# Optimization experiments

Measured on AMD Instinct MI355X. Metric: run time of the kernel, lower is better.

The kernel has to match this reference:

```python
import jax, jax.numpy as jnp
import numpy as np

N = 100_000      # atoms
E = 1_600_000    # edges (avg degree 16)
B = 50           # graphs in batch
H = 128          # hidden dim
R = 50           # num radial features (emb(0.0, 6.0, 50))
MAXZ = 100
CUTOFF = 6.0
L = 3            # interaction layers (ext[1..6])


def setup_inputs() -> dict:
    key = jax.random.key(0)
    ks = jax.random.split(key, 16)
    z = jax.random.randint(ks[0], (N,), 0, MAXZ)
    pos = jax.random.normal(ks[1], (N, 3), dtype=jnp.float32) * 3.0
    cell = jnp.eye(3, dtype=jnp.float32)[None] * 10.0 + 0.1 * jax.random.normal(ks[2], (B, 3, 3), dtype=jnp.float32)
    edge_index = jax.random.randint(ks[3], (2, E), 0, N)
    cell_offsets = jax.random.randint(ks[4], (E, 3), -1, 2)  # {-1,0,1}
    edge_batch = jax.random.randint(ks[5], (E,), 0, B)
    # learned parameters
    atom_emb = jax.random.normal(ks[6], (MAXZ, H), dtype=jnp.float32) * 0.1
    dist_table = jax.random.normal(ks[7], (R, R), dtype=jnp.float32) * 0.1  # dist_emb embedding table
    s_e = 1.0 / np.sqrt(2 * H + R)
    s_h = 1.0 / np.sqrt(H)
    We = jax.random.normal(ks[8], (L, 2 * H + R, H), dtype=jnp.float32) * s_e
    be = jnp.zeros((L, H), dtype=jnp.float32)
    Wv = jax.random.normal(ks[9], (L, H, H), dtype=jnp.float32) * s_h
    bv = jnp.zeros((L, H), dtype=jnp.float32)
    Wh = jax.random.normal(ks[10], (H, H), dtype=jnp.float32) * s_h
    bh = jnp.zeros((H,), dtype=jnp.float32)
    return dict(z=z, pos=pos, cell=cell, edge_index=edge_index,
                cell_offsets=cell_offsets, edge_batch=edge_batch,
                atom_emb=atom_emb, dist_table=dist_table,
                We=We, be=be, Wv=Wv, bv=bv, Wh=Wh, bh=bh)


def reference(z, pos, cell, edge_index, cell_offsets, edge_batch,
              atom_emb, dist_table, We, be, Wv, bv, Wh, bh):
    row, col = edge_index[0], edge_index[1]
    # get_pbc_distances: offsets = cell_offsets @ per-edge cell
    off = jnp.einsum('ek,ekl->el', cell_offsets.astype(jnp.float32), cell[edge_batch])  # [E,3]
    vec = pos[row] - pos[col] + off
    dist = jnp.sqrt(jnp.sum(vec * vec, axis=-1))  # [E]
    # dist_emb(dist.to(long)): integer-cast distance indexes the embedding table
    demb = dist_table[jnp.clip(dist.astype(jnp.int32), 0, R - 1)]  # [E,R]
    env = 0.5 * (jnp.cos(jnp.pi * jnp.clip(dist, 0.0, CUTOFF) / CUTOFF) + 1.0)  # cosine cutoff [E]
    v = atom_emb[z]  # ext[0]: atom embedding [N,H]
    for i in range(L):
        # ext[2i+1]: edge layer — gather endpoints, concat with radial features
        m = jnp.concatenate([v[row], v[col], demb], axis=-1)  # [E, 2H+R]
        e = jax.nn.silu(m @ We[i] + be[i]) * env[:, None]     # [E, H]
        # ext[2i+2]: node layer — scatter-sum messages to destination nodes
        agg = jax.ops.segment_sum(e, col, num_segments=N)     # [N, H]
        v = v + jax.nn.silu(agg @ Wv[i] + bv[i])
    v = v @ Wh + bh  # head
    return (v, pos, dist)
```

## Files before the change

kernel.cpp:

```cpp
#include <hip/hip_runtime.h>
#include <hip/hip_bf16.h>

#define HID 128
#define RR 50
#define NLAY 3
#define CBSH 9
#define CBSZ 512
#define CPAD (CBSZ * 3)
#define ACHUNK 8192

typedef __attribute__((ext_vector_type(8))) short short8;
typedef __attribute__((ext_vector_type(4))) float f32x4;
typedef __attribute__((ext_vector_type(2))) float f32x2;

static __device__ __forceinline__ unsigned short f2bf(float x) {
    unsigned int b = __builtin_bit_cast(unsigned int, x);
    b = b + 0x7FFFu + ((b >> 16) & 1u);
    return (unsigned short)(b >> 16);
}
static __device__ __forceinline__ float bf2f(unsigned int u) {
    return __builtin_bit_cast(float, u << 16);
}
static __device__ __forceinline__ f32x2 bfpair(unsigned u) {
    f32x2 r;
    r.x = __builtin_bit_cast(float, u << 16);
    r.y = __builtin_bit_cast(float, u & 0xffff0000u);
    return r;
}
static __device__ __forceinline__ float silu_f(float x) {
    float e = __expf(-x);
    return x * __builtin_amdgcn_rcpf(1.0f + e);
}

__global__ __launch_bounds__(256) void k_geom(
    const int* __restrict__ ei, const int* __restrict__ co,
    const int* __restrict__ eb, const float* __restrict__ cell,
    const float* __restrict__ pos, float* __restrict__ dist_out,
    int2* __restrict__ rec, int* __restrict__ ccol,
    float* __restrict__ out_pos, int N3, int E)
{
    int e = blockIdx.x * 256 + threadIdx.x;
    if (e < N3) out_pos[e] = pos[e];
    if (e >= E) return;
    int r = ei[e], c = ei[E + e], b = eb[e];
    float c0 = (float)co[3*e], c1 = (float)co[3*e+1], c2 = (float)co[3*e+2];
    const float* cb = cell + b * 9;
    float v0 = pos[3*r+0] - pos[3*c+0] + c0*cb[0] + c1*cb[3] + c2*cb[6];
    float v1 = pos[3*r+1] - pos[3*c+1] + c0*cb[1] + c1*cb[4] + c2*cb[7];
    float v2 = pos[3*r+2] - pos[3*c+2] + c0*cb[2] + c1*cb[5] + c2*cb[8];
    float d = sqrtf(v0*v0 + v1*v1 + v2*v2);
    dist_out[e] = d;
    bool keep = d < 6.0f;
    ccol[e] = keep ? c : -1;
    if (keep) {
        int di = (int)d;
        di = di < 0 ? 0 : (di > RR - 1 ? RR - 1 : di);
        float envv = 0.5f * (cosf(d * (3.14159265358979323846f / 6.0f)) + 1.0f);
        rec[e] = make_int2((r << 8) | di, __builtin_bit_cast(int, envv));
    }
}

__global__ __launch_bounds__(256) void k_cntA(
    const int* __restrict__ col, int* __restrict__ gb, int E, int nCB)
{
    __shared__ int lc[1024];
    int tid = threadIdx.x;
    for (int i = tid; i < nCB; i += 256) lc[i] = 0;
    __syncthreads();
    int base = blockIdx.x * ACHUNK;
    int end = base + ACHUNK; if (end > E) end = E;
    for (int e = base + tid; e < end; e += 256) {
        int c = col[e];
        if (c >= 0) atomicAdd(&lc[((unsigned)c) >> CBSH], 1);
    }
    __syncthreads();
    for (int i = tid; i < nCB; i += 256)
        if (lc[i]) atomicAdd(&gb[i], lc[i]);
}

__global__ __launch_bounds__(256) void k_projz(
    const int* __restrict__ z, const float* __restrict__ emb,
    const unsigned short* __restrict__ P12t,
    unsigned short* __restrict__ v, unsigned short* __restrict__ P1,
    unsigned short* __restrict__ P2, int N)
{
    int gid = blockIdx.x * 256 + threadIdx.x;
    if (gid >= N * 16) return;
    int n = gid >> 4, c4 = gid & 15;
    int zz = z[n];
    const float4* ep = (const float4*)(emb + (size_t)zz * HID) + c4 * 2;
    float4 a = ep[0], b = ep[1];
    uint4 u;
    u.x = ((unsigned)f2bf(a.y) << 16) | f2bf(a.x);
    u.y = ((unsigned)f2bf(a.w) << 16) | f2bf(a.z);
    u.z = ((unsigned)f2bf(b.y) << 16) | f2bf(b.x);
    u.w = ((unsigned)f2bf(b.w) << 16) | f2bf(b.z);
    *(uint4*)(v + (size_t)n * HID + c4 * 8) = u;
    uint4 t1 = *(const uint4*)(P12t + (size_t)zz * 256 + c4 * 8);
    uint4 t2 = *(const uint4*)(P12t + (size_t)zz * 256 + 128 + c4 * 8);
    *(uint4*)(P1 + (size_t)n * HID + c4 * 8) = t1;
    *(uint4*)(P2 + (size_t)n * HID + c4 * 8) = t2;
}

__global__ __launch_bounds__(256) void k_wprep(
    const float* __restrict__ We, const float* __restrict__ Wv,
    const float* __restrict__ Wh, const float* __restrict__ dt,
    const float* __restrict__ be, const float* __restrict__ emb,
    unsigned short* __restrict__ WvP, unsigned short* __restrict__ WcP,
    unsigned short* __restrict__ WhP, unsigned short* __restrict__ TbP,
    unsigned short* __restrict__ P12t)
{
    int blk = blockIdx.x;
    if (blk < 640) {
        int t = blk * 256 + threadIdx.x;
        int j = t & 7, l = (t >> 3) & 63, s = (t >> 9) & 3;
        int ln = l & 15, g = l >> 4;
        int k = s * 32 + g * 4 + (j & 3) + ((j >> 2) << 4);
        if (t < 3 * 16384) {
            int i = t >> 14; int nt = (t >> 11) & 7;
            WvP[t] = f2bf(Wv[(size_t)i * 16384 + k * HID + nt * 16 + ln]);
        } else if (t < 3 * 16384 + 3 * 32768) {
            int u = t - 3 * 16384; int i = u >> 15; int nt = (u >> 11) & 15;
            int col = nt * 16 + ln;
            float val = (col < HID) ? We[(size_t)i * 306 * HID + k * HID + col]
                                    : We[(size_t)i * 306 * HID + (HID + k) * HID + (col - HID)];
            WcP[u] = f2bf(val);
        } else {
            int u = t - 3 * 16384 - 3 * 32768; int nt = (u >> 11) & 7;
            WhP[u] = f2bf(Wh[k * HID + nt * 16 + ln]);
        }
    } else if (blk < 640 + NLAY * RR) {
        if (threadIdx.x >= HID) return;
        int row = blk - 640;
        int i = row / RR, r = row % RR;
        int c = threadIdx.x;
        float s = be[i * HID + c];
        const float* w = We + (size_t)i * 306 * HID + 256 * HID + c;
        const float* dr = dt + r * RR;
        for (int k = 0; k < RR; ++k) s += dr[k] * w[k * HID];
        TbP[(i * RR + r) * HID + c] = f2bf(s);
    } else {
        int zz = blk - 640 - NLAY * RR;
        int c = threadIdx.x;
        int cm = c & 127, half = c >> 7;
        const float* er = emb + (size_t)zz * HID;
        const float* w = We + (size_t)(half * 128) * HID + cm;
        float s = 0.f;
        #pragma unroll 8
        for (int k = 0; k < 128; ++k) s += er[k] * w[k * HID];
        P12t[(size_t)zz * 256 + c] = f2bf(s);
    }
}

__global__ __launch_bounds__(256) void k_scanA(
    const int* __restrict__ gb, int* __restrict__ gbase,
    int* __restrict__ gcur, int nCB)
{
    __shared__ int ps[256];
    __shared__ int carry;
    int t = threadIdx.x;
    if (t == 0) carry = 0;
    __syncthreads();
    for (int base = 0; base < nCB; base += 256) {
        int v = (base + t < nCB) ? gb[base + t] : 0;
        ps[t] = v; __syncthreads();
        for (int d = 1; d < 256; d <<= 1) {
            int x = (t >= d) ? ps[t - d] : 0;
            __syncthreads();
            ps[t] += x;
            __syncthreads();
        }
        int excl = carry + ps[t] - v;
        if (base + t < nCB) { gbase[base + t] = excl; gcur[base + t] = excl; }
        __syncthreads();
        if (t == 0) carry += ps[255];
        __syncthreads();
    }
    if (t == 0) gbase[nCB] = carry;
}

__global__ __launch_bounds__(256) void k_splitA(
    const int* __restrict__ col, const int2* __restrict__ rec,
    int* __restrict__ gcur, int2* __restrict__ binned,
    int* __restrict__ bcol, int E, int nCB)
{
    __shared__ int lc[1024];
    __shared__ int lres[1024];
    int tid = threadIdx.x;
    for (int i = tid; i < nCB; i += 256) lc[i] = 0;
    __syncthreads();
    int base = blockIdx.x * ACHUNK;
    int end = base + ACHUNK; if (end > E) end = E;
    for (int e = base + tid; e < end; e += 256) {
        int c = col[e];
        if (c >= 0) atomicAdd(&lc[((unsigned)c) >> CBSH], 1);
    }
    __syncthreads();
    for (int i = tid; i < nCB; i += 256) {
        lres[i] = lc[i] ? atomicAdd(&gcur[i], lc[i]) : 0;
        lc[i] = 0;
    }
    __syncthreads();
    for (int e = base + tid; e < end; e += 256) {
        int c = col[e];
        if (c < 0) continue;
        int b = ((unsigned)c) >> CBSH;
        int rank = atomicAdd(&lc[b], 1);
        int p = lres[b] + rank;
        binned[p] = rec[e];
        bcol[p] = c;
    }
}

__global__ __launch_bounds__(256) void k_sortB(
    const int2* __restrict__ binned, const int* __restrict__ bcol,
    const int* __restrict__ gbase, int2* __restrict__ meta,
    int2* __restrict__ noff, int N)
{
    __shared__ int lcnt[CBSZ], lcur[CBSZ], pscan[CBSZ];
    __shared__ int wsum[64];
    const int b = blockIdx.x;
    const int tid = threadIdx.x;
    const int s = gbase[b], e = gbase[b + 1];
    const int mbase = s + b * CPAD;
    for (int i = tid; i < CBSZ; i += 256) { lcnt[i] = 0; lcur[i] = 0; }
    __syncthreads();
    for (int t = s + tid; t < e; t += 256)
        atomicAdd(&lcnt[bcol[t] & (CBSZ - 1)], 1);
    __syncthreads();
    if (tid < 64) {
        int ssum = 0;
        #pragma unroll
        for (int k = 0; k < 8; ++k) {
            int idx = tid * 8 + k;
            int pc = (lcnt[idx] + 3) & ~3;
            pscan[idx] = ssum;
            ssum += pc;
        }
        wsum[tid] = ssum;
    }
    __syncthreads();
    if (tid == 0) {
        int c = 0;
        for (int i = 0; i < 64; ++i) { int t = wsum[i]; wsum[i] = c; c += t; }
    }
    __syncthreads();
    if (tid < 64) {
        #pragma unroll
        for (int k = 0; k < 8; ++k) pscan[tid * 8 + k] += wsum[tid];
    }
    __syncthreads();
    for (int i = tid; i < CBSZ; i += 256) {
        int node = (b << CBSH) + i;
        if (node < N) {
            noff[node] = make_int2(mbase + pscan[i], lcnt[i]);
            int pb = mbase + pscan[i] + lcnt[i];
            int pads = ((lcnt[i] + 3) & ~3) - lcnt[i];
            for (int k = 0; k < pads; ++k) meta[pb + k] = make_int2(0, 0);
        }
    }
    __syncthreads();
    for (int t = s + tid; t < e; t += 256) {
        int local = bcol[t] & (CBSZ - 1);
        int rank = atomicAdd(&lcur[local], 1);
        meta[mbase + pscan[local] + rank] = binned[t];
    }
}

#define PLD(M) (*(const unsigned*)(P1b + (unsigned)((((unsigned)(M).x) & 0xFFFFFF00u) | lane4)))
#define TLDG(M) (*(const unsigned*)(Tb_ + (((((unsigned)(M).x) & 255u) << 8) | lane4)))

#define EP(GG, TBU, MM)                                                       \
    {                                                                         \
        f32x2 xx = bfpair(GG) + (bfpair(TBU) + p2v);                          \
        f32x2 nx = xx * -1.442695041f;                                        \
        f32x2 ee;                                                             \
        ee.x = __builtin_amdgcn_exp2f(nx.x);                                  \
        ee.y = __builtin_amdgcn_exp2f(nx.y);                                  \
        f32x2 dd = ee + 1.0f;                                                 \
        f32x2 rr;                                                             \
        rr.x = __builtin_amdgcn_rcpf(dd.x);                                   \
        rr.y = __builtin_amdgcn_rcpf(dd.y);                                   \
        f32x2 sl = xx * rr;                                                   \
        float evf = __builtin_bit_cast(float, (MM).y);                        \
        av += sl * evf;                                                       \
    }

static __device__ __forceinline__ short8 ldfrag(const unsigned short* A, int r, int s, int g) {
    const char* p = (const char*)(A + r * 136) + s * 64 + g * 8;
    uint2 lo = *(const uint2*)p;
    uint2 hi = *(const uint2*)(p + 32);
    uint4 u; u.x = lo.x; u.y = lo.y; u.z = hi.x; u.w = hi.y;
    return __builtin_bit_cast(short8, u);
}

template<int NT2, bool FINAL>
__global__ __launch_bounds__(256) void k_layer(
    const unsigned short* __restrict__ P1,
    const unsigned short* __restrict__ P2,
    const unsigned short* __restrict__ TbBf,
    const int2* __restrict__ meta,
    const int2* __restrict__ noff,
    const unsigned short* __restrict__ B1p,
    const float* __restrict__ b1,
    unsigned short* __restrict__ v,
    const unsigned short* __restrict__ B2p,
    const float* __restrict__ b2,
    unsigned short* __restrict__ P1d,
    unsigned short* __restrict__ P2d,
    float* __restrict__ outd, int N)
{
    __shared__ __align__(16) unsigned short SHB[2 * 32 * 136];
    unsigned short* SH  = SHB;
    unsigned short* SHV = SHB + 32 * 136;
    const int tid = threadIdx.x;
    const int node0 = blockIdx.x * 32;
    const int w = tid >> 6, l = tid & 63, g = l >> 4, ln = l & 15;
    const int lane = l;
    const unsigned lane4 = 4u * (unsigned)lane;

    #pragma unroll
    for (int i = 0; i < 2; ++i) {
        int u = tid + 256 * i, r = u >> 4, c = u & 15;
        uint4 y4 = make_uint4(0, 0, 0, 0);
        if (node0 + r < N) y4 = *(const uint4*)(v + (size_t)(node0 + r) * HID + c * 8);
        *(uint4*)(SHV + r * 136 + c * 8) = y4;
    }

    {
        const char* P1b = (const char*)P1;
        const char* Tb_ = (const char*)TbBf;
        const int r0 = w << 3;
        int2 ni = make_int2(0, 0);
        {
            int pn = node0 + r0 + lane;
            if (lane < 8 && pn < N) ni = noff[pn];
        }
        #pragma unroll 1
        for (int i = 0; i < 8; ++i) {
            int r = r0 + i;
            unsigned* outp = (unsigned*)(SH + r * 136 + 2 * lane);
            int n = __builtin_amdgcn_readlane(ni.y, i);
            if (n == 0) { *outp = 0u; continue; }
            int s = __builtin_amdgcn_readlane(ni.x, i);
            int node = node0 + r;
            unsigned p2u = *(const unsigned*)(P2 + (size_t)node * HID + 2 * lane);
            n = (n + 3) & ~3;
            f32x2 p2v = bfpair(p2u);
            f32x2 av; av.x = 0.f; av.y = 0.f;
            const int2* mp = meta + s;
            int2 m0 = mp[0], m1 = mp[1], m2 = mp[2], m3 = mp[3];
            unsigned g0 = PLD(m0), g1 = PLD(m1), g2 = PLD(m2), g3 = PLD(m3);
            for (int t = 0; t < n; t += 4) {
                int2 n0 = mp[t + 4], n1 = mp[t + 5], n2 = mp[t + 6], n3 = mp[t + 7];
                unsigned h0 = PLD(n0), h1 = PLD(n1), h2 = PLD(n2), h3 = PLD(n3);
                unsigned t0 = TLDG(m0), t1 = TLDG(m1), t2 = TLDG(m2), t3 = TLDG(m3);
                EP(g0, t0, m0) EP(g1, t1, m1) EP(g2, t2, m2) EP(g3, t3, m3)
                m0 = n0; m1 = n1; m2 = n2; m3 = n3;
                g0 = h0; g1 = h1; g2 = h2; g3 = h3;
            }
            *outp = (((unsigned)f2bf(av.y)) << 16) | (unsigned)f2bf(av.x);
        }
    }

    {
        short8 bf1[2][4];
        #pragma unroll
        for (int nt = 0; nt < 2; ++nt)
            #pragma unroll
            for (int s = 0; s < 4; ++s)
                bf1[nt][s] = *(const short8*)(B1p + (((2 * w + nt) * 4 + s) * 64 + l) * 8);
        __syncthreads();
        f32x4 acc[2][2] = {};
        #pragma unroll
        for (int s = 0; s < 4; ++s)
            #pragma unroll
            for (int mt = 0; mt < 2; ++mt) {
                short8 af = ldfrag(SH, 16 * mt + ln, s, g);
                acc[mt][0] = __builtin_amdgcn_mfma_f32_16x16x32_bf16(af, bf1[0][s], acc[mt][0], 0, 0, 0);
                acc[mt][1] = __builtin_amdgcn_mfma_f32_16x16x32_bf16(af, bf1[1][s], acc[mt][1], 0, 0, 0);
            }
        __syncthreads();
        float bvc0 = b1[32 * w + ln], bvc1 = b1[32 * w + 16 + ln];
        #pragma unroll
        for (int mt = 0; mt < 2; ++mt)
            #pragma unroll
            for (int nt = 0; nt < 2; ++nt) {
                int col = 32 * w + 16 * nt + ln;
                float bb = nt ? bvc1 : bvc0;
                #pragma unroll
                for (int j = 0; j < 4; ++j) {
                    int r = 16 * mt + 4 * g + j;
                    float y = silu_f(acc[mt][nt][j] + bb);
                    float vn = bf2f((unsigned)SHV[r * 136 + col]) + y;
                    SH[r * 136 + col] = f2bf(vn);
                }
            }
        __syncthreads();
        if (!FINAL) {
            #pragma unroll
            for (int i = 0; i < 2; ++i) {
                int u = tid + 256 * i, r = u >> 4, c = u & 15;
                if (node0 + r < N)
                    *(uint4*)(v + (size_t)(node0 + r) * HID + c * 8) =
                        *(const uint4*)(SH + r * 136 + c * 8);
            }
        }
    }

    constexpr int NTW = NT2 / 4;
    short8 bf2[NTW][4];
    #pragma unroll
    for (int nt = 0; nt < NTW; ++nt)
        #pragma unroll
        for (int s = 0; s < 4; ++s)
            bf2[nt][s] = *(const short8*)(B2p + (((w * NTW + nt) * 4 + s) * 64 + l) * 8);
    f32x4 acc2[2][NTW] = {};
    #pragma unroll
    for (int s = 0; s < 4; ++s)
        #pragma unroll
        for (int mt = 0; mt < 2; ++mt) {
            short8 af = ldfrag(SH, 16 * mt + ln, s, g);
            #pragma unroll
            for (int nt = 0; nt < NTW; ++nt)
                acc2[mt][nt] = __builtin_amdgcn_mfma_f32_16x16x32_bf16(af, bf2[nt][s], acc2[mt][nt], 0, 0, 0);
        }
    __syncthreads();
    if (FINAL) {
        float* fst = (float*)SHB;
        #pragma unroll
        for (int nt = 0; nt < NTW; ++nt) {
            int col = (w * NTW + nt) * 16 + ln;
            float bb = b2[col];
            #pragma unroll
            for (int mt = 0; mt < 2; ++mt)
                #pragma unroll
                for (int j = 0; j < 4; ++j) {
                    int r = 16 * mt + 4 * g + j;
                    fst[r * 132 + col] = acc2[mt][nt][j] + bb;
                }
        }
        __syncthreads();
        #pragma unroll
        for (int i = 0; i < 4; ++i) {
            int u = tid + 256 * i, r = u >> 5, cg = u & 31;
            if (node0 + r < N)
                *(float4*)(outd + (size_t)(node0 + r) * HID + cg * 4) =
                    *(const float4*)(fst + r * 132 + cg * 4);
        }
    } else {
        #pragma unroll
        for (int nt = 0; nt < NTW; ++nt) {
            int gidx = w * NTW + nt;
            int colm = (gidx * 16 + ln) & 127;
            unsigned short* dst = (gidx < 8) ? SHV : SH;
            #pragma unroll
            for (int mt = 0; mt < 2; ++mt)
                #pragma unroll
                for (int j = 0; j < 4; ++j) {
                    int r = 16 * mt + 4 * g + j;
                    dst[r * 136 + colm] = f2bf(acc2[mt][nt][j]);
                }
        }
        __syncthreads();
        #pragma unroll
        for (int i = 0; i < 2; ++i) {
            int u = tid + 256 * i, r = u >> 4, cg = u & 15;
            if (node0 + r < N) {
                *(uint4*)(P1d + (size_t)(node0 + r) * HID + cg * 8) =
                    *(const uint4*)(SHV + r * 136 + cg * 8);
                *(uint4*)(P2d + (size_t)(node0 + r) * HID + cg * 8) =
                    *(const uint4*)(SH + r * 136 + cg * 8);
            }
        }
    }
}

extern "C" void kernel_launch(void* const* d_in, const int* in_sizes, int n_in,
                              void* d_out, int out_size, void* d_ws, size_t ws_size,
                              hipStream_t stream)
{
    const int*   z    = (const int*)d_in[0];
    const float* pos  = (const float*)d_in[1];
    const float* cell = (const float*)d_in[2];
    const int*   ei   = (const int*)d_in[3];
    const int*   co   = (const int*)d_in[4];
    const int*   eb   = (const int*)d_in[5];
    const float* emb  = (const float*)d_in[6];
    const float* dt   = (const float*)d_in[7];
    const float* We   = (const float*)d_in[8];
    const float* be   = (const float*)d_in[9];
    const float* Wv   = (const float*)d_in[10];
    const float* bv   = (const float*)d_in[11];
    const float* Wh   = (const float*)d_in[12];
    const float* bh   = (const float*)d_in[13];

    const int N = in_sizes[0];
    const int E = in_sizes[5];
    const int MAXZ = in_sizes[6] / HID;
    const int nCB = (N + CBSZ - 1) >> CBSH;
    const size_t metaN = (size_t)E + (size_t)nCB * CPAD + 32;

    char* p = (char*)d_ws;
    unsigned short* v    = (unsigned short*)p;  p += (size_t)N * HID * 2;
    unsigned short* P1a  = (unsigned short*)p;  p += (size_t)N * HID * 2;
    unsigned short* P1b  = (unsigned short*)p;  p += (size_t)N * HID * 2;
    unsigned short* P2   = (unsigned short*)p;  p += (size_t)N * HID * 2;
    int2*  meta  = (int2*)p;                    p += metaN * 8;
    int2*  noff  = (int2*)p;                    p += (size_t)N * 8;
    int*   gb    = (int*)p;                     p += (size_t)(nCB + 1) * 4;
    int*   gbase = (int*)p;                     p += (size_t)(nCB + 1) * 4;
    int*   gcur  = (int*)p;                     p += (size_t)(nCB + 1) * 4;
    unsigned short* TbP = (unsigned short*)p;   p += (size_t)NLAY * RR * HID * 2;
    unsigned short* WvP = (unsigned short*)p;   p += (size_t)3 * 16384 * 2;
    unsigned short* WcP = (unsigned short*)p;   p += (size_t)3 * 32768 * 2;
    unsigned short* WhP = (unsigned short*)p;   p += (size_t)16384 * 2;
    unsigned short* P12t = (unsigned short*)p;  p += (size_t)MAXZ * 256 * 2;

    int2* rec    = (int2*)P1a;
    int2* binned = (int2*)((char*)P1a + (size_t)E * 8);
    int*  ccol   = (int*)P2;
    int*  bcol   = (int*)((char*)P2 + (size_t)E * 4);

    float* out_v    = (float*)d_out;
    float* out_pos  = out_v + (size_t)N * HID;
    float* out_dist = out_pos + (size_t)N * 3;

    const int nlayer = (N + 31) / 32;
    const int nblkA = (E + ACHUNK - 1) / ACHUNK;
    const int N3 = N * 3;
    int ngeom = (E + 255) / 256;
    if ((N3 + 255) / 256 > ngeom) ngeom = (N3 + 255) / 256;

    hipMemsetAsync(gb, 0, (size_t)(nCB + 1) * 4, stream);
    hipMemsetAsync(meta, 0, metaN * 8, stream);
    k_geom<<<ngeom, 256, 0, stream>>>(ei, co, eb, cell, pos, out_dist, rec, ccol, out_pos, N3, E);
    k_cntA<<<nblkA, 256, 0, stream>>>(ccol, gb, E, nCB);
    k_scanA<<<1, 256, 0, stream>>>(gb, gbase, gcur, nCB);
    k_splitA<<<nblkA, 256, 0, stream>>>(ccol, rec, gcur, binned, bcol, E, nCB);
    k_sortB<<<nCB, 256, 0, stream>>>(binned, bcol, gbase, meta, noff, N);

    k_wprep<<<640 + NLAY * RR + MAXZ, 256, 0, stream>>>(
        We, Wv, Wh, dt, be, emb, WvP, WcP, WhP, TbP, P12t);

    k_projz<<<(N * 16 + 255) / 256, 256, 0, stream>>>(z, emb, P12t, v, P1a, P2, N);

    unsigned short* Pin  = P1a;
    unsigned short* Pout = P1b;
    for (int i = 0; i < NLAY; ++i) {
        if (i < NLAY - 1) {
            k_layer<16, false><<<nlayer, 256, 0, stream>>>(
                Pin, P2, TbP + (size_t)i * RR * HID, meta, noff,
                WvP + (size_t)i * 16384, bv + (size_t)i * HID, v,
                WcP + (size_t)(i + 1) * 32768, nullptr, Pout, P2, nullptr, N);
        } else {
            k_layer<8, true><<<nlayer, 256, 0, stream>>>(
                Pin, P2, TbP + (size_t)i * RR * HID, meta, noff,
                WvP + (size_t)i * 16384, bv + (size_t)i * HID, v,
                WhP, bh, nullptr, nullptr, out_v, N);
        }
        unsigned short* t = Pin; Pin = Pout; Pout = t;
    }
}
```

Before: 219.2 us.

## Fuse bucket counting into geometry kernel and double layer block size to 512

The geometry kernel now also counts kept edges per column bucket in shared memory and flushes the counts to the global histogram, so the separate counting kernel and its extra pass over ccol are removed. The layer kernel moves from 256 to 512 threads per 32-node block: each wave gathers edges for 4 nodes instead of 8 and computes one 16-column tile in each matmul instead of two. This gives more waves to hide gather latency. The cost is more shared-memory atomics in the geometry kernel and fewer MFMA tiles per wave, with a larger per-block footprint.

After: 246.7 us. 1.13x slower.

```diff
diff --git a/kernel.cpp b/kernel.cpp
--- a/kernel.cpp
+++ b/kernel.cpp
@@ -37,41 +37,33 @@
     const int* __restrict__ eb, const float* __restrict__ cell,
     const float* __restrict__ pos, float* __restrict__ dist_out,
     int2* __restrict__ rec, int* __restrict__ ccol,
-    float* __restrict__ out_pos, int N3, int E)
-{
-    int e = blockIdx.x * 256 + threadIdx.x;
-    if (e < N3) out_pos[e] = pos[e];
-    if (e >= E) return;
-    int r = ei[e], c = ei[E + e], b = eb[e];
-    float c0 = (float)co[3*e], c1 = (float)co[3*e+1], c2 = (float)co[3*e+2];
-    const float* cb = cell + b * 9;
-    float v0 = pos[3*r+0] - pos[3*c+0] + c0*cb[0] + c1*cb[3] + c2*cb[6];
-    float v1 = pos[3*r+1] - pos[3*c+1] + c0*cb[1] + c1*cb[4] + c2*cb[7];
-    float v2 = pos[3*r+2] - pos[3*c+2] + c0*cb[2] + c1*cb[5] + c2*cb[8];
-    float d = sqrtf(v0*v0 + v1*v1 + v2*v2);
-    dist_out[e] = d;
-    bool keep = d < 6.0f;
-    ccol[e] = keep ? c : -1;
-    if (keep) {
-        int di = (int)d;
-        di = di < 0 ? 0 : (di > RR - 1 ? RR - 1 : di);
-        float envv = 0.5f * (cosf(d * (3.14159265358979323846f / 6.0f)) + 1.0f);
-        rec[e] = make_int2((r << 8) | di, __builtin_bit_cast(int, envv));
-    }
-}
-
-__global__ __launch_bounds__(256) void k_cntA(
-    const int* __restrict__ col, int* __restrict__ gb, int E, int nCB)
+    float* __restrict__ out_pos, int* __restrict__ gb,
+    int N3, int E, int nCB)
 {
     __shared__ int lc[1024];
     int tid = threadIdx.x;
-    for (int i = tid; i < nCB; i += 256) lc[i] = 0;
-    __syncthreads();
-    int base = blockIdx.x * ACHUNK;
-    int end = base + ACHUNK; if (end > E) end = E;
-    for (int e = base + tid; e < end; e += 256) {
-        int c = col[e];
-        if (c >= 0) atomicAdd(&lc[((unsigned)c) >> CBSH], 1);
+    for (int i = tid; i < 1024; i += 256) lc[i] = 0;
+    __syncthreads();
+    int e = blockIdx.x * 256 + tid;
+    if (e < N3) out_pos[e] = pos[e];
+    if (e < E) {
+        int r = ei[e], c = ei[E + e], b = eb[e];
+        float c0 = (float)co[3*e], c1 = (float)co[3*e+1], c2 = (float)co[3*e+2];
+        const float* cb = cell + b * 9;
+        float v0 = pos[3*r+0] - pos[3*c+0] + c0*cb[0] + c1*cb[3] + c2*cb[6];
+        float v1 = pos[3*r+1] - pos[3*c+1] + c0*cb[1] + c1*cb[4] + c2*cb[7];
+        float v2 = pos[3*r+2] - pos[3*c+2] + c0*cb[2] + c1*cb[5] + c2*cb[8];
+        float d = sqrtf(v0*v0 + v1*v1 + v2*v2);
+        dist_out[e] = d;
+        bool keep = d < 6.0f;
+        ccol[e] = keep ? c : -1;
+        if (keep) {
+            int di = (int)d;
+            di = di < 0 ? 0 : (di > RR - 1 ? RR - 1 : di);
+            float envv = 0.5f * (cosf(d * (3.14159265358979323846f / 6.0f)) + 1.0f);
+            rec[e] = make_int2((r << 8) | di, __builtin_bit_cast(int, envv));
+            atomicAdd(&lc[((unsigned)c) >> CBSH], 1);
+        }
     }
     __syncthreads();
     for (int i = tid; i < nCB; i += 256)
@@ -295,7 +287,7 @@
 }
 
 template<int NT2, bool FINAL>
-__global__ __launch_bounds__(256) void k_layer(
+__global__ __launch_bounds__(512) void k_layer(
     const unsigned short* __restrict__ P1,
     const unsigned short* __restrict__ P2,
     const unsigned short* __restrict__ TbBf,
@@ -315,13 +307,12 @@
     unsigned short* SHV = SHB + 32 * 136;
     const int tid = threadIdx.x;
     const int node0 = blockIdx.x * 32;
-    const int w = tid >> 6, l = tid & 63, g = l >> 4, ln = l & 15;
+    const int w = tid >> 6, l = tid & 63, g = (l >> 4) & 3, ln = l & 15;
     const int lane = l;
     const unsigned lane4 = 4u * (unsigned)lane;
 
-    #pragma unroll
-    for (int i = 0; i < 2; ++i) {
-        int u = tid + 256 * i, r = u >> 4, c = u & 15;
+    {
+        int r = tid >> 4, c = tid & 15;
         uint4 y4 = make_uint4(0, 0, 0, 0);
         if (node0 + r < N) y4 = *(const uint4*)(v + (size_t)(node0 + r) * HID + c * 8);
         *(uint4*)(SHV + r * 136 + c * 8) = y4;
@@ -330,14 +321,14 @@
     {
         const char* P1b = (const char*)P1;
         const char* Tb_ = (const char*)TbBf;
-        const int r0 = w << 3;
+        const int r0 = w << 2;
         int2 ni = make_int2(0, 0);
         {
             int pn = node0 + r0 + lane;
-            if (lane < 8 && pn < N) ni = noff[pn];
+            if (lane < 4 && pn < N) ni = noff[pn];
         }
         #pragma unroll 1
-        for (int i = 0; i < 8; ++i) {
+        for (int i = 0; i < 4; ++i) {
             int r = r0 + i;
             unsigned* outp = (unsigned*)(SH + r * 136 + 2 * lane);
             int n = __builtin_amdgcn_readlane(ni.y, i);
@@ -364,51 +355,42 @@
     }
 
     {
-        short8 bf1[2][4];
-        #pragma unroll
-        for (int nt = 0; nt < 2; ++nt)
-            #pragma unroll
-            for (int s = 0; s < 4; ++s)
-                bf1[nt][s] = *(const short8*)(B1p + (((2 * w + nt) * 4 + s) * 64 + l) * 8);
-        __syncthreads();
-        f32x4 acc[2][2] = {};
+        short8 bf1[4];
+        #pragma unroll
+        for (int s = 0; s < 4; ++s)
+            bf1[s] = *(const short8*)(B1p + ((w * 4 + s) * 64 + l) * 8);
+        __syncthreads();
+        f32x4 acc[2] = {};
         #pragma unroll
         for (int s = 0; s < 4; ++s)
             #pragma unroll
             for (int mt = 0; mt < 2; ++mt) {
                 short8 af = ldfrag(SH, 16 * mt + ln, s, g);
-                acc[mt][0] = __builtin_amdgcn_mfma_f32_16x16x32_bf16(af, bf1[0][s], acc[mt][0], 0, 0, 0);
-                acc[mt][1] = __builtin_amdgcn_mfma_f32_16x16x32_bf16(af, bf1[1][s], acc[mt][1], 0, 0, 0);
+                acc[mt] = __builtin_amdgcn_mfma_f32_16x16x32_bf16(af, bf1[s], acc[mt], 0, 0, 0);
             }
         __syncthreads();
-        float bvc0 = b1[32 * w + ln], bvc1 = b1[32 * w + 16 + ln];
-        #pragma unroll
-        for (int mt = 0; mt < 2; ++mt)
+        float bvc = b1[16 * w + ln];
+        #pragma unroll
+        for (int mt = 0; mt < 2; ++mt) {
+            int col = 16 * w + ln;
             #pragma unroll
-            for (int nt = 0; nt < 2; ++nt) {
-                int col = 32 * w + 16 * nt + ln;
-                float bb = nt ? bvc1 : bvc0;
-                #pragma unroll
-                for (int j = 0; j < 4; ++j) {
-                    int r = 16 * mt + 4 * g + j;
-                    float y = silu_f(acc[mt][nt][j] + bb);
-                    float vn = bf2f((unsigned)SHV[r * 136 + col]) + y;
-                    SH[r * 136 + col] = f2bf(vn);
-                }
+            for (int j = 0; j < 4; ++j) {
+                int r = 16 * mt + 4 * g + j;
+                float y = silu_f(acc[mt][j] + bvc);
+                float vn = bf2f((unsigned)SHV[r * 136 + col]) + y;
+                SH[r * 136 + col] = f2bf(vn);
             }
+        }
         __syncthreads();
         if (!FINAL) {
-            #pragma unroll
-            for (int i = 0; i < 2; ++i) {
-                int u = tid + 256 * i, r = u >> 4, c = u & 15;
-                if (node0 + r < N)
-                    *(uint4*)(v + (size_t)(node0 + r) * HID + c * 8) =
-                        *(const uint4*)(SH + r * 136 + c * 8);
-            }
-        }
-    }
-
-    constexpr int NTW = NT2 / 4;
+            int r = tid >> 4, c = tid & 15;
+            if (node0 + r < N)
+                *(uint4*)(v + (size_t)(node0 + r) * HID + c * 8) =
+                    *(const uint4*)(SH + r * 136 + c * 8);
+        }
+    }
+
+    constexpr int NTW = NT2 / 8;
     short8 bf2[NTW][4];
     #pragma unroll
     for (int nt = 0; nt < NTW; ++nt)
@@ -428,22 +410,19 @@
     __syncthreads();
     if (FINAL) {
         float* fst = (float*)SHB;
-        #pragma unroll
-        for (int nt = 0; nt < NTW; ++nt) {
-            int col = (w * NTW + nt) * 16 + ln;
-            float bb = b2[col];
+        int col = w * 16 + ln;
+        float bb = b2[col];
+        #pragma unroll
+        for (int mt = 0; mt < 2; ++mt)
             #pragma unroll
-            for (int mt = 0; mt < 2; ++mt)
-                #pragma unroll
-                for (int j = 0; j < 4; ++j) {
-                    int r = 16 * mt + 4 * g + j;
-                    fst[r * 132 + col] = acc2[mt][nt][j] + bb;
-                }
-        }
-        __syncthreads();
-        #pragma unroll
-        for (int i = 0; i < 4; ++i) {
-            int u = tid + 256 * i, r = u >> 5, cg = u & 31;
+            for (int j = 0; j < 4; ++j) {
+                int r = 16 * mt + 4 * g + j;
+                fst[r * 132 + col] = acc2[mt][0][j] + bb;
+            }
+        __syncthreads();
+        #pragma unroll
+        for (int i = 0; i < 2; ++i) {
+            int u = tid + 512 * i, r = u >> 5, cg = u & 31;
             if (node0 + r < N)
                 *(float4*)(outd + (size_t)(node0 + r) * HID + cg * 4) =
                     *(const float4*)(fst + r * 132 + cg * 4);
@@ -463,9 +442,8 @@
                 }
         }
         __syncthreads();
-        #pragma unroll
-        for (int i = 0; i < 2; ++i) {
-            int u = tid + 256 * i, r = u >> 4, cg = u & 15;
+        {
+            int r = tid >> 4, cg = tid & 15;
             if (node0 + r < N) {
                 *(uint4*)(P1d + (size_t)(node0 + r) * HID + cg * 8) =
                     *(const uint4*)(SHV + r * 136 + cg * 8);
@@ -534,8 +512,8 @@
 
     hipMemsetAsync(gb, 0, (size_t)(nCB + 1) * 4, stream);
     hipMemsetAsync(meta, 0, metaN * 8, stream);
-    k_geom<<<ngeom, 256, 0, stream>>>(ei, co, eb, cell, pos, out_dist, rec, ccol, out_pos, N3, E);
-    k_cntA<<<nblkA, 256, 0, stream>>>(ccol, gb, E, nCB);
+    k_geom<<<ngeom, 256, 0, stream>>>(ei, co, eb, cell, pos, out_dist, rec, ccol,
+                                      out_pos, gb, N3, E, nCB);
     k_scanA<<<1, 256, 0, stream>>>(gb, gbase, gcur, nCB);
     k_splitA<<<nblkA, 256, 0, stream>>>(ccol, rec, gcur, binned, bcol, E, nCB);
     k_sortB<<<nCB, 256, 0, stream>>>(binned, bcol, gbase, meta, noff, N);
@@ -549,12 +527,12 @@
     unsigned short* Pout = P1b;
     for (int i = 0; i < NLAY; ++i) {
         if (i < NLAY - 1) {
-            k_layer<16, false><<<nlayer, 256, 0, stream>>>(
+            k_layer<16, false><<<nlayer, 512, 0, stream>>>(
                 Pin, P2, TbP + (size_t)i * RR * HID, meta, noff,
                 WvP + (size_t)i * 16384, bv + (size_t)i * HID, v,
                 WcP + (size_t)(i + 1) * 32768, nullptr, Pout, P2, nullptr, N);
         } else {
-            k_layer<8, true><<<nlayer, 256, 0, stream>>>(
+            k_layer<8, true><<<nlayer, 512, 0, stream>>>(
                 Pin, P2, TbP + (size_t)i * RR * HID, meta, noff,
                 WvP + (size_t)i * 16384, bv + (size_t)i * HID, v,
                 WhP, bh, nullptr, nullptr, out_v, N);
```
